# Kernel optimization log

Measured on AMD Instinct MI355X. Metric: run time of the kernel, lower is better.

The kernel has to match this reference:

```python
import jax, jax.numpy as jnp
import numpy as np

CUTOFF = 5.0

def ssp(x):
    # shifted softplus: ln(0.5*e^x + 0.5)
    return jax.nn.softplus(x) - jnp.log(2.0).astype(x.dtype)

def cosine_cutoff(r):
    return 0.5 * (jnp.cos(jnp.pi * r / CUTOFF) + 1.0) * (r < CUTOFF).astype(r.dtype)

def setup_inputs() -> dict:
    key = jax.random.key(0)
    ks = jax.random.split(key, 16)
    B, A, N, Nd, F, Din, Dout, Th = 2, 512, 1024, 64, 64, 128, 128, 25
    inp = {}
    inp['x'] = jax.random.normal(ks[0], (B, A, Din), dtype=jnp.float32)
    inp['r_double'] = jax.random.uniform(ks[1], (B, A, Nd), dtype=jnp.float32)
    inp['r_ij'] = jax.random.uniform(ks[2], (B, A, N), dtype=jnp.float32)
    inp['r_ik'] = jax.random.uniform(ks[3], (B, A, N), dtype=jnp.float32)
    inp['r_jk'] = jax.random.uniform(ks[4], (B, A, N), dtype=jnp.float32)
    inp['neighbors'] = jax.random.randint(ks[5], (B, A, Nd), 0, A, dtype=jnp.int32)
    inp['neighbor_mask'] = jnp.ones((B, A, Nd), dtype=jnp.float32)
    inp['neighbors_j'] = jax.random.randint(ks[6], (B, A, N), 0, A, dtype=jnp.int32)
    inp['neighbors_k'] = jax.random.randint(ks[7], (B, A, N), 0, A, dtype=jnp.int32)
    inp['triple_masks'] = jnp.ones((B, A, N), dtype=jnp.float32)
    inp['d_ijk'] = jax.random.uniform(ks[8], (B, A, N, Th), dtype=jnp.float32)
    s = 0.1
    inp['W_in2f'] = s * jax.random.normal(ks[9], (Din, F), dtype=jnp.float32)
    inp['W_t1'] = s * jax.random.normal(ks[10], (Th, F), dtype=jnp.float32)
    inp['b_t1'] = jnp.zeros((F,), dtype=jnp.float32)
    inp['W_t2'] = s * jax.random.normal(ks[11], (F, F), dtype=jnp.float32)
    inp['b_t2'] = jnp.zeros((F,), dtype=jnp.float32)
    inp['W_f2out'] = s * jax.random.normal(ks[12], (F, Dout), dtype=jnp.float32)
    inp['b_f2out'] = jnp.zeros((Dout,), dtype=jnp.float32)
    return inp

def reference(x, r_double, r_ij, r_ik, r_jk, neighbors, neighbor_mask,
              neighbors_j, neighbors_k, triple_masks, d_ijk,
              W_in2f, W_t1, b_t1, W_t2, b_t2, W_f2out, b_f2out):
    # Triple filter: 2-layer MLP on angular basis, modulated by cutoffs
    h = ssp(jnp.einsum('bant,tf->banf', d_ijk, W_t1) + b_t1)
    W_triple = jnp.einsum('banf,fg->bang', h, W_t2) + b_t2
    W_triple = W_triple * cosine_cutoff(r_ij)[..., None] * cosine_cutoff(r_ik)[..., None]

    # in2f: (B, A, F)
    y = jnp.einsum('bad,df->baf', x, W_in2f)
    B, A, N = neighbors_j.shape
    F = y.shape[-1]
    # gather neighbor features along atom axis
    yj = jnp.take_along_axis(y, neighbors_j.reshape(B, A * N, 1), axis=1).reshape(B, A, N, F)
    yk = jnp.take_along_axis(y, neighbors_k.reshape(B, A * N, 1), axis=1).reshape(B, A, N, F)
    w_ij = r_ij[..., None]
    w_ik = r_ik[..., None]
    y = (w_ij * yj + w_ik * yk) / (w_ij + w_ik)
    # filter multiply + masked sum aggregation over triples axis
    y = y * W_triple
    y = jnp.sum(y * triple_masks[..., None], axis=2)
    # f2out with shifted-softplus activation
    out = ssp(jnp.einsum('baf,fo->bao', y, W_f2out) + b_f2out)
    return out
```

## Files before the change

### kernel.cpp

```cpp
#include <hip/hip_runtime.h>
#include <hip/hip_fp16.h>

#define BB 2
#define AA 512
#define NN 1024
#define FF 64
#define DIN 128
#define DOUT 128
#define TH 25
#define ASTRIDE 40
#define HSTRIDE 72
#define NSPLIT 4

typedef _Float16 half8 __attribute__((ext_vector_type(8)));
typedef _Float16 half4v __attribute__((ext_vector_type(4)));
typedef float floatx4 __attribute__((ext_vector_type(4)));

__device__ __forceinline__ float ssp_f(float x) {
    return __logf(0.5f * __expf(x) + 0.5f);
}

__device__ __forceinline__ float cutcos(float r) {
    float c = 0.5f * (__cosf(r * (3.14159265358979323846f / 5.0f)) + 1.0f);
    return (r < 5.0f) ? c : 0.0f;
}

__device__ __forceinline__ __half2 ssp2(__half2 x) {
    const __half2 hlf = __float2half2_rn(0.5f);
    return h2log(__hfma2(h2exp(x), hlf, hlf));
}

__device__ __forceinline__ __half2 pk2(float a, float b) {
    auto v = __builtin_amdgcn_cvt_pkrtz(a, b);
    __half2 r;
    __builtin_memcpy(&r, &v, sizeof(r));
    return r;
}

__device__ __forceinline__ half4v pack4(__half2 lo, __half2 hi) {
    half4v r;
    __builtin_memcpy(&r, &lo, 4);
    __builtin_memcpy(reinterpret_cast<char*>(&r) + 4, &hi, 4);
    return r;
}

#define OFF_Y       0
#define OFF_PARTIAL (OFF_Y + (size_t)BB * AA * FF * 2)
#define OFF_B1      (OFF_PARTIAL + (size_t)NSPLIT * BB * AA * FF * 4)
#define OFF_B2      (OFF_B1 + 4 * 64 * 8 * 2)
#define OFF_BP      (OFF_B2 + 8 * 64 * 8 * 2)

__global__ void in2f_prep_kernel(const float* __restrict__ x,
                                 const float* __restrict__ Wi,
                                 _Float16* __restrict__ y,
                                 const float* __restrict__ W_t1, const float* __restrict__ b_t1,
                                 const float* __restrict__ W_t2, const float* __restrict__ b_t2,
                                 _Float16* __restrict__ B1tab, _Float16* __restrict__ B2tab,
                                 _Float16* __restrict__ BPtab) {
    __shared__ float xs[DIN];
    const int ba = blockIdx.x;
    const int t = threadIdx.x;
    xs[t] = x[ba * DIN + t];
    xs[t + 64] = x[ba * DIN + 64 + t];
    __syncthreads();
    float acc = 0.f;
#pragma unroll 8
    for (int d = 0; d < DIN; ++d) acc += xs[d] * Wi[d * FF + t];
    y[ba * FF + t] = (_Float16)acc;

    if (ba == 0) {
        const int lane = t, quad = t >> 4, l16 = t & 15;
#pragma unroll
        for (int g = 0; g < 4; ++g) {
#pragma unroll
            for (int j = 0; j < 8; ++j) {
                int k = quad * 8 + j;
                B1tab[(g * 64 + lane) * 8 + j] =
                    (k < TH) ? (_Float16)W_t1[k * FF + g * 16 + l16] : (_Float16)0.f;
            }
#pragma unroll
            for (int e = 0; e < 2; ++e) {
                BPtab[((g * 2 + e) * 64 + lane) * 2 + 0] =
                    (_Float16)b_t1[g * 16 + quad * 4 + 2 * e];
                BPtab[((g * 2 + e) * 64 + lane) * 2 + 1] =
                    (_Float16)b_t1[g * 16 + quad * 4 + 2 * e + 1];
                BPtab[1024 + ((g * 2 + e) * 64 + lane) * 2 + 0] =
                    (_Float16)b_t2[g * 16 + quad * 4 + 2 * e];
                BPtab[1024 + ((g * 2 + e) * 64 + lane) * 2 + 1] =
                    (_Float16)b_t2[g * 16 + quad * 4 + 2 * e + 1];
            }
#pragma unroll
            for (int q = 0; q < 2; ++q)
#pragma unroll
                for (int j = 0; j < 8; ++j)
                    B2tab[((g * 2 + q) * 64 + lane) * 8 + j] =
                        (_Float16)W_t2[(q * 32 + quad * 8 + j) * FF + g * 16 + l16];
        }
    }
}

__global__ __launch_bounds__(256) void triple_kernel(
    const int* __restrict__ nbrj, const int* __restrict__ nbrk,
    const float* __restrict__ r_ij, const float* __restrict__ r_ik,
    const float* __restrict__ tmask, const float* __restrict__ d_ijk,
    const _Float16* __restrict__ B1tab, const _Float16* __restrict__ B2tab,
    const _Float16* __restrict__ BPtab,
    const _Float16* __restrict__ y_tab, float* __restrict__ partial) {

    __shared__ __align__(16) _Float16 a_tile[4][16 * ASTRIDE];
    __shared__ __align__(16) _Float16 h_tile[4][16 * HSTRIDE];
    __shared__ float red[4][FF];

    const int blk = blockIdx.x;
    const int ba = blk >> 2;
    const int split = blk & 3;
    const int b = ba >> 9;
    const int tid = threadIdx.x;
    const int w = tid >> 6;
    const int lane = tid & 63;
    const int quad = lane >> 4;
    const int l16 = lane & 15;
    const int rA = lane >> 3;
    const int fc = (lane & 7) * 8;

    const long ban = (long)ba * NN;
    const float* dbase = d_ijk + (long)ba * NN * TH;
    const _Float16* yb = y_tab + (long)b * (AA * FF);

    half8 B1[4];
    half8 B2[4][2];
    __half2 b1p[4][2], b2p[4][2];
#pragma unroll
    for (int g = 0; g < 4; ++g) {
        B1[g] = *(const half8*)(B1tab + (g * 64 + lane) * 8);
        B2[g][0] = *(const half8*)(B2tab + ((g * 2 + 0) * 64 + lane) * 8);
        B2[g][1] = *(const half8*)(B2tab + ((g * 2 + 1) * 64 + lane) * 8);
#pragma unroll
        for (int e = 0; e < 2; ++e) {
            b1p[g][e] = *(const __half2*)(BPtab + ((g * 2 + e) * 64 + lane) * 2);
            b2p[g][e] = *(const __half2*)(BPtab + 1024 + ((g * 2 + e) * 64 + lane) * 2);
        }
    }

    const int myn = (split * 16 + quad * 4 + w) * 16 + l16;
    const long myna = ban + myn;
    const float rijL = r_ij[myna], rikL = r_ik[myna];
    const float ivL = cutcos(rijL) * cutcos(rikL) * tmask[myna] / (rijL + rikL);
    const float wjf = rijL * ivL, wkf = rikL * ivL;
    const int pjL = nbrj[myna], pkL = nbrk[myna];

    for (int idx = lane; idx < 16 * 7; idx += 64) {
        int r = idx / 7, c = 25 + idx % 7;
        a_tile[w][r * ASTRIDE + c] = (_Float16)0.f;
    }

    int lofs2[3][2];
#pragma unroll
    for (int m = 0; m < 3; ++m)
#pragma unroll
        for (int e = 0; e < 2; ++e) {
            int s = m * 128 + lane * 2 + e;
            int r = s / TH, c = s - r * TH;
            lofs2[m][e] = r * ASTRIDE + c;
        }
    const int tofs = 15 * ASTRIDE + 9 + lane;

    float acc[8];
#pragma unroll
    for (int i = 0; i < 8; ++i) acc[i] = 0.f;
    const floatx4 zero4 = {0.f, 0.f, 0.f, 0.f};

    float2 pA[3];
    float pT = 0.f;
    {
        const int n0 = (split * 16 + w) * 16;
        const float* dsrc = dbase + n0 * TH;
#pragma unroll
        for (int m = 0; m < 3; ++m) pA[m] = *(const float2*)(dsrc + m * 128 + lane * 2);
        if (lane < 16) pT = dsrc[384 + lane];
    }

#pragma unroll 1
    for (int it = 0; it < NN / (16 * 4 * NSPLIT); ++it) {
        const int sl0 = it * 16 + rA;
        const int sl1 = sl0 + 8;
        const int pj0 = __shfl(pjL, sl0), pk0 = __shfl(pkL, sl0);
        const int pj1 = __shfl(pjL, sl1), pk1 = __shfl(pkL, sl1);
        half8 gj0 = *(const half8*)(yb + pj0 * FF + fc);
        half8 gk0 = *(const half8*)(yb + pk0 * FF + fc);
        half8 gj1 = *(const half8*)(yb + pj1 * FF + fc);
        half8 gk1 = *(const half8*)(yb + pk1 * FF + fc);

#pragma unroll
        for (int m = 0; m < 3; ++m) {
            a_tile[w][lofs2[m][0]] = (_Float16)pA[m].x;
            a_tile[w][lofs2[m][1]] = (_Float16)pA[m].y;
        }
        if (lane < 16) a_tile[w][tofs] = (_Float16)pT;

        if (it + 1 < NN / (16 * 4 * NSPLIT)) {
            const int n0 = (split * 16 + (it + 1) * 4 + w) * 16;
            const float* dn = dbase + n0 * TH;
#pragma unroll
            for (int m = 0; m < 3; ++m) pA[m] = *(const float2*)(dn + m * 128 + lane * 2);
            if (lane < 16) pT = dn[384 + lane];
        }

        const __half2 wj0 = __float2half2_rn(__shfl(wjf, sl0));
        const __half2 wk0 = __float2half2_rn(__shfl(wkf, sl0));
        const __half2 wj1 = __float2half2_rn(__shfl(wjf, sl1));
        const __half2 wk1 = __float2half2_rn(__shfl(wkf, sl1));

        half8 afrag = *(const half8*)&a_tile[w][l16 * ASTRIDE + quad * 8];
#pragma unroll
        for (int g = 0; g < 4; ++g) {
            floatx4 hv = __builtin_amdgcn_mfma_f32_16x16x32_f16(B1[g], afrag, zero4, 0, 0, 0);
            __half2 h01 = ssp2(__hadd2(pk2(hv[0], hv[1]), b1p[g][0]));
            __half2 h23 = ssp2(__hadd2(pk2(hv[2], hv[3]), b1p[g][1]));
            *(half4v*)&h_tile[w][l16 * HSTRIDE + g * 16 + quad * 4] = pack4(h01, h23);
        }

        half8 a2q0 = *(const half8*)&h_tile[w][l16 * HSTRIDE + quad * 8];
        half8 a2q1 = *(const half8*)&h_tile[w][l16 * HSTRIDE + 32 + quad * 8];
#pragma unroll
        for (int g = 0; g < 4; ++g) {
            floatx4 w2 = __builtin_amdgcn_mfma_f32_16x16x32_f16(B2[g][0], a2q0, zero4, 0, 0, 0);
            w2 = __builtin_amdgcn_mfma_f32_16x16x32_f16(B2[g][1], a2q1, w2, 0, 0, 0);
            __half2 f01 = __hadd2(pk2(w2[0], w2[1]), b2p[g][0]);
            __half2 f23 = __hadd2(pk2(w2[2], w2[3]), b2p[g][1]);
            *(half4v*)&h_tile[w][l16 * HSTRIDE + g * 16 + quad * 4] = pack4(f01, f23);
        }
        half8 f0 = *(const half8*)&h_tile[w][rA * HSTRIDE + fc];
        half8 f1 = *(const half8*)&h_tile[w][(8 + rA) * HSTRIDE + fc];

        const __half2* gj0p = (const __half2*)&gj0;
        const __half2* gk0p = (const __half2*)&gk0;
        const __half2* gj1p = (const __half2*)&gj1;
        const __half2* gk1p = (const __half2*)&gk1;
        const __half2* f0p = (const __half2*)&f0;
        const __half2* f1p = (const __half2*)&f1;
#pragma unroll
        for (int p = 0; p < 4; ++p) {
            __half2 fv0 = __hfma2(wj0, gj0p[p], __hmul2(wk0, gk0p[p]));
            __half2 fv1 = __hfma2(wj1, gj1p[p], __hmul2(wk1, gk1p[p]));
            __half2 tot = __hfma2(f1p[p], fv1, __hmul2(f0p[p], fv0));
            acc[2 * p]     += __low2float(tot);
            acc[2 * p + 1] += __high2float(tot);
        }
    }

#pragma unroll
    for (int i = 0; i < 8; ++i) {
        acc[i] += __shfl_xor(acc[i], 8, 64);
        acc[i] += __shfl_xor(acc[i], 16, 64);
        acc[i] += __shfl_xor(acc[i], 32, 64);
    }
    if (lane < 8)
#pragma unroll
        for (int i = 0; i < 8; ++i) red[w][lane * 8 + i] = acc[i];
    __syncthreads();

    if (tid < FF)
        partial[(split * (BB * AA) + ba) * FF + tid] =
            red[0][tid] + red[1][tid] + red[2][tid] + red[3][tid];
}

__global__ void out_kernel(const float* __restrict__ partial,
                           const float* __restrict__ Wf,
                           const float* __restrict__ bf,
                           float* __restrict__ out) {
    __shared__ float yag[FF];
    const int ba = blockIdx.x;
    const int t = threadIdx.x;
    if (t < FF) {
        float s = 0.f;
#pragma unroll
        for (int sp = 0; sp < NSPLIT; ++sp)
            s += partial[(sp * (BB * AA) + ba) * FF + t];
        yag[t] = s;
    }
    __syncthreads();
    float a = bf[t];
#pragma unroll 8
    for (int f = 0; f < FF; ++f) a += yag[f] * Wf[f * DOUT + t];
    out[(long)ba * DOUT + t] = ssp_f(a);
}

extern "C" void kernel_launch(void* const* d_in, const int* in_sizes, int n_in,
                              void* d_out, int out_size, void* d_ws, size_t ws_size,
                              hipStream_t stream) {
    const float* x       = (const float*)d_in[0];
    const float* r_ij    = (const float*)d_in[2];
    const float* r_ik    = (const float*)d_in[3];
    const int*   nbrj    = (const int*)d_in[7];
    const int*   nbrk    = (const int*)d_in[8];
    const float* tmask   = (const float*)d_in[9];
    const float* d_ijk   = (const float*)d_in[10];
    const float* W_in2f  = (const float*)d_in[11];
    const float* W_t1    = (const float*)d_in[12];
    const float* b_t1    = (const float*)d_in[13];
    const float* W_t2    = (const float*)d_in[14];
    const float* b_t2    = (const float*)d_in[15];
    const float* W_f2out = (const float*)d_in[16];
    const float* b_f2out = (const float*)d_in[17];
    float* out = (float*)d_out;

    char* ws = (char*)d_ws;
    _Float16* y      = (_Float16*)(ws + OFF_Y);
    float* partial   = (float*)(ws + OFF_PARTIAL);
    _Float16* B1tab  = (_Float16*)(ws + OFF_B1);
    _Float16* B2tab  = (_Float16*)(ws + OFF_B2);
    _Float16* BPtab  = (_Float16*)(ws + OFF_BP);

    in2f_prep_kernel<<<BB * AA, 64, 0, stream>>>(x, W_in2f, y, W_t1, b_t1,
                                                 W_t2, b_t2, B1tab, B2tab, BPtab);
    triple_kernel<<<BB * AA * NSPLIT, 256, 0, stream>>>(nbrj, nbrk, r_ij, r_ik,
                                                        tmask, d_ijk, B1tab, B2tab,
                                                        BPtab, y, partial);
    out_kernel<<<BB * AA, 128, 0, stream>>>(partial, W_f2out, b_f2out, out);
}
```

Measured before the change: 239.1 us.

## Keep MFMA fragments in registers, removing LDS staging of MLP tiles

The first-layer weight columns are permuted so that the MFMA output fragment of layer one directly forms the B-operand fragment of layer two. This lets the hidden activations stay in registers instead of round-tripping through LDS tiles. The d_ijk input is loaded straight from global memory into the A fragment, and neighbor gathers use the MFMA output layout so the filter multiply happens in fp32 per lane. The loop is fully unrolled with double-buffered prefetch, at the cost of more registers and a longer shuffle reduction.

```diff
diff --git a/kernel.cpp b/kernel.cpp
--- a/kernel.cpp
+++ b/kernel.cpp
@@ -8,9 +8,8 @@
 #define DIN 128
 #define DOUT 128
 #define TH 25
-#define ASTRIDE 40
-#define HSTRIDE 72
 #define NSPLIT 4
+#define NIT 4
 
 typedef _Float16 half8 __attribute__((ext_vector_type(8)));
 typedef _Float16 half4v __attribute__((ext_vector_type(4)));
@@ -37,10 +36,12 @@
     return r;
 }
 
-__device__ __forceinline__ half4v pack4(__half2 lo, __half2 hi) {
-    half4v r;
-    __builtin_memcpy(&r, &lo, 4);
-    __builtin_memcpy(reinterpret_cast<char*>(&r) + 4, &hi, 4);
+__device__ __forceinline__ half8 pack8(__half2 a, __half2 b, __half2 c, __half2 d) {
+    half8 r;
+    __builtin_memcpy(reinterpret_cast<char*>(&r) + 0,  &a, 4);
+    __builtin_memcpy(reinterpret_cast<char*>(&r) + 4,  &b, 4);
+    __builtin_memcpy(reinterpret_cast<char*>(&r) + 8,  &c, 4);
+    __builtin_memcpy(reinterpret_cast<char*>(&r) + 12, &d, 4);
     return r;
 }
 
@@ -48,7 +49,8 @@
 #define OFF_PARTIAL (OFF_Y + (size_t)BB * AA * FF * 2)
 #define OFF_B1      (OFF_PARTIAL + (size_t)NSPLIT * BB * AA * FF * 4)
 #define OFF_B2      (OFF_B1 + 4 * 64 * 8 * 2)
-#define OFF_BP      (OFF_B2 + 8 * 64 * 8 * 2)
+#define OFF_B1P     (OFF_B2 + 8 * 64 * 8 * 2)
+#define OFF_B2F     (OFF_B1P + 4 * 2 * 64 * 2 * 2)
 
 __global__ void in2f_prep_kernel(const float* __restrict__ x,
                                  const float* __restrict__ Wi,
@@ -56,7 +58,7 @@
                                  const float* __restrict__ W_t1, const float* __restrict__ b_t1,
                                  const float* __restrict__ W_t2, const float* __restrict__ b_t2,
                                  _Float16* __restrict__ B1tab, _Float16* __restrict__ B2tab,
-                                 _Float16* __restrict__ BPtab) {
+                                 _Float16* __restrict__ B1Ptab, float* __restrict__ B2Ftab) {
     __shared__ float xs[DIN];
     const int ba = blockIdx.x;
     const int t = threadIdx.x;
@@ -70,24 +72,22 @@
 
     if (ba == 0) {
         const int lane = t, quad = t >> 4, l16 = t & 15;
-#pragma unroll
-        for (int g = 0; g < 4; ++g) {
+        const int baseg[4] = {0, 4, 32, 36};
+#pragma unroll
+        for (int g = 0; g < 4; ++g) {
+            const int feat_m = baseg[g] + 8 * (l16 >> 2) + (l16 & 3);
 #pragma unroll
             for (int j = 0; j < 8; ++j) {
                 int k = quad * 8 + j;
                 B1tab[(g * 64 + lane) * 8 + j] =
-                    (k < TH) ? (_Float16)W_t1[k * FF + g * 16 + l16] : (_Float16)0.f;
+                    (k < TH) ? (_Float16)W_t1[k * FF + feat_m] : (_Float16)0.f;
             }
 #pragma unroll
             for (int e = 0; e < 2; ++e) {
-                BPtab[((g * 2 + e) * 64 + lane) * 2 + 0] =
-                    (_Float16)b_t1[g * 16 + quad * 4 + 2 * e];
-                BPtab[((g * 2 + e) * 64 + lane) * 2 + 1] =
-                    (_Float16)b_t1[g * 16 + quad * 4 + 2 * e + 1];
-                BPtab[1024 + ((g * 2 + e) * 64 + lane) * 2 + 0] =
-                    (_Float16)b_t2[g * 16 + quad * 4 + 2 * e];
-                BPtab[1024 + ((g * 2 + e) * 64 + lane) * 2 + 1] =
-                    (_Float16)b_t2[g * 16 + quad * 4 + 2 * e + 1];
+                B1Ptab[((g * 2 + e) * 64 + lane) * 2 + 0] =
+                    (_Float16)b_t1[baseg[g] + 8 * quad + 2 * e];
+                B1Ptab[((g * 2 + e) * 64 + lane) * 2 + 1] =
+                    (_Float16)b_t1[baseg[g] + 8 * quad + 2 * e + 1];
             }
 #pragma unroll
             for (int q = 0; q < 2; ++q)
@@ -95,6 +95,9 @@
                 for (int j = 0; j < 8; ++j)
                     B2tab[((g * 2 + q) * 64 + lane) * 8 + j] =
                         (_Float16)W_t2[(q * 32 + quad * 8 + j) * FF + g * 16 + l16];
+#pragma unroll
+            for (int r = 0; r < 4; ++r)
+                B2Ftab[lane * 16 + g * 4 + r] = b_t2[g * 16 + 4 * quad + r];
         }
     }
 }
@@ -104,12 +107,10 @@
     const float* __restrict__ r_ij, const float* __restrict__ r_ik,
     const float* __restrict__ tmask, const float* __restrict__ d_ijk,
     const _Float16* __restrict__ B1tab, const _Float16* __restrict__ B2tab,
-    const _Float16* __restrict__ BPtab,
+    const _Float16* __restrict__ B1Ptab, const float* __restrict__ B2Ftab,
     const _Float16* __restrict__ y_tab, float* __restrict__ partial) {
 
-    __shared__ __align__(16) _Float16 a_tile[4][16 * ASTRIDE];
-    __shared__ __align__(16) _Float16 h_tile[4][16 * HSTRIDE];
-    __shared__ float red[4][FF];
+    __shared__ __align__(16) float red[4][FF];
 
     const int blk = blockIdx.x;
     const int ba = blk >> 2;
@@ -120,8 +121,6 @@
     const int lane = tid & 63;
     const int quad = lane >> 4;
     const int l16 = lane & 15;
-    const int rA = lane >> 3;
-    const int fc = (lane & 7) * 8;
 
     const long ban = (long)ba * NN;
     const float* dbase = d_ijk + (long)ba * NN * TH;
@@ -129,135 +128,118 @@
 
     half8 B1[4];
     half8 B2[4][2];
-    __half2 b1p[4][2], b2p[4][2];
+    __half2 b1p[4][2];
+    floatx4 b2f[4];
 #pragma unroll
     for (int g = 0; g < 4; ++g) {
         B1[g] = *(const half8*)(B1tab + (g * 64 + lane) * 8);
         B2[g][0] = *(const half8*)(B2tab + ((g * 2 + 0) * 64 + lane) * 8);
         B2[g][1] = *(const half8*)(B2tab + ((g * 2 + 1) * 64 + lane) * 8);
-#pragma unroll
-        for (int e = 0; e < 2; ++e) {
-            b1p[g][e] = *(const __half2*)(BPtab + ((g * 2 + e) * 64 + lane) * 2);
-            b2p[g][e] = *(const __half2*)(BPtab + 1024 + ((g * 2 + e) * 64 + lane) * 2);
-        }
+        b1p[g][0] = *(const __half2*)(B1Ptab + ((g * 2 + 0) * 64 + lane) * 2);
+        b1p[g][1] = *(const __half2*)(B1Ptab + ((g * 2 + 1) * 64 + lane) * 2);
+        b2f[g] = *(const floatx4*)(B2Ftab + lane * 16 + g * 4);
     }
 
     const int myn = (split * 16 + quad * 4 + w) * 16 + l16;
     const long myna = ban + myn;
     const float rijL = r_ij[myna], rikL = r_ik[myna];
     const float ivL = cutcos(rijL) * cutcos(rikL) * tmask[myna] / (rijL + rikL);
-    const float wjf = rijL * ivL, wkf = rikL * ivL;
+    const float wjL = rijL * ivL, wkL = rikL * ivL;
     const int pjL = nbrj[myna], pkL = nbrk[myna];
 
-    for (int idx = lane; idx < 16 * 7; idx += 64) {
-        int r = idx / 7, c = 25 + idx % 7;
-        a_tile[w][r * ASTRIDE + c] = (_Float16)0.f;
-    }
-
-    int lofs2[3][2];
-#pragma unroll
-    for (int m = 0; m < 3; ++m)
-#pragma unroll
-        for (int e = 0; e < 2; ++e) {
-            int s = m * 128 + lane * 2 + e;
-            int r = s / TH, c = s - r * TH;
-            lofs2[m][e] = r * ASTRIDE + c;
-        }
-    const int tofs = 15 * ASTRIDE + 9 + lane;
-
-    float acc[8];
-#pragma unroll
-    for (int i = 0; i < 8; ++i) acc[i] = 0.f;
+    const float* dp0 = dbase + (long)((split * 16 + w) * 16 + l16) * TH + quad * 8;
+    const bool qok = (quad < 3);
+
+    float acc[16];
+#pragma unroll
+    for (int i = 0; i < 16; ++i) acc[i] = 0.f;
     const floatx4 zero4 = {0.f, 0.f, 0.f, 0.f};
 
-    float2 pA[3];
-    float pT = 0.f;
+    float dv[2][8];
+    half4v gj[2][4], gk[2][4];
+    float wjc[2], wkc[2];
+
     {
-        const int n0 = (split * 16 + w) * 16;
-        const float* dsrc = dbase + n0 * TH;
-#pragma unroll
-        for (int m = 0; m < 3; ++m) pA[m] = *(const float2*)(dsrc + m * 128 + lane * 2);
-        if (lane < 16) pT = dsrc[384 + lane];
-    }
-
-#pragma unroll 1
-    for (int it = 0; it < NN / (16 * 4 * NSPLIT); ++it) {
-        const int sl0 = it * 16 + rA;
-        const int sl1 = sl0 + 8;
-        const int pj0 = __shfl(pjL, sl0), pk0 = __shfl(pkL, sl0);
-        const int pj1 = __shfl(pjL, sl1), pk1 = __shfl(pkL, sl1);
-        half8 gj0 = *(const half8*)(yb + pj0 * FF + fc);
-        half8 gk0 = *(const half8*)(yb + pk0 * FF + fc);
-        half8 gj1 = *(const half8*)(yb + pj1 * FF + fc);
-        half8 gk1 = *(const half8*)(yb + pk1 * FF + fc);
-
-#pragma unroll
-        for (int m = 0; m < 3; ++m) {
-            a_tile[w][lofs2[m][0]] = (_Float16)pA[m].x;
-            a_tile[w][lofs2[m][1]] = (_Float16)pA[m].y;
-        }
-        if (lane < 16) a_tile[w][tofs] = (_Float16)pT;
-
-        if (it + 1 < NN / (16 * 4 * NSPLIT)) {
-            const int n0 = (split * 16 + (it + 1) * 4 + w) * 16;
-            const float* dn = dbase + n0 * TH;
-#pragma unroll
-            for (int m = 0; m < 3; ++m) pA[m] = *(const float2*)(dn + m * 128 + lane * 2);
-            if (lane < 16) pT = dn[384 + lane];
-        }
-
-        const __half2 wj0 = __float2half2_rn(__shfl(wjf, sl0));
-        const __half2 wk0 = __float2half2_rn(__shfl(wkf, sl0));
-        const __half2 wj1 = __float2half2_rn(__shfl(wjf, sl1));
-        const __half2 wk1 = __float2half2_rn(__shfl(wkf, sl1));
-
-        half8 afrag = *(const half8*)&a_tile[w][l16 * ASTRIDE + quad * 8];
-#pragma unroll
-        for (int g = 0; g < 4; ++g) {
-            floatx4 hv = __builtin_amdgcn_mfma_f32_16x16x32_f16(B1[g], afrag, zero4, 0, 0, 0);
-            __half2 h01 = ssp2(__hadd2(pk2(hv[0], hv[1]), b1p[g][0]));
-            __half2 h23 = ssp2(__hadd2(pk2(hv[2], hv[3]), b1p[g][1]));
-            *(half4v*)&h_tile[w][l16 * HSTRIDE + g * 16 + quad * 4] = pack4(h01, h23);
-        }
-
-        half8 a2q0 = *(const half8*)&h_tile[w][l16 * HSTRIDE + quad * 8];
-        half8 a2q1 = *(const half8*)&h_tile[w][l16 * HSTRIDE + 32 + quad * 8];
+        const int sl = l16;
+        const int pj = __shfl(pjL, sl), pk = __shfl(pkL, sl);
+        wjc[0] = __shfl(wjL, sl);
+        wkc[0] = __shfl(wkL, sl);
+        const _Float16* pjb = yb + pj * FF + quad * 4;
+        const _Float16* pkb = yb + pk * FF + quad * 4;
+#pragma unroll
+        for (int g = 0; g < 4; ++g) {
+            gj[0][g] = *(const half4v*)(pjb + g * 16);
+            gk[0][g] = *(const half4v*)(pkb + g * 16);
+        }
+        dv[0][0] = dp0[0];
+#pragma unroll
+        for (int j = 1; j < 8; ++j) dv[0][j] = qok ? dp0[j] : 0.f;
+    }
+
+#pragma unroll
+    for (int it = 0; it < NIT; ++it) {
+        const int cur = it & 1, nxt = cur ^ 1;
+
+        if (it + 1 < NIT) {
+            const int sl = (it + 1) * 16 + l16;
+            const int pj = __shfl(pjL, sl), pk = __shfl(pkL, sl);
+            wjc[nxt] = __shfl(wjL, sl);
+            wkc[nxt] = __shfl(wkL, sl);
+            const _Float16* pjb = yb + pj * FF + quad * 4;
+            const _Float16* pkb = yb + pk * FF + quad * 4;
+#pragma unroll
+            for (int g = 0; g < 4; ++g) {
+                gj[nxt][g] = *(const half4v*)(pjb + g * 16);
+                gk[nxt][g] = *(const half4v*)(pkb + g * 16);
+            }
+            const float* dp = dp0 + (it + 1) * 1600;
+            dv[nxt][0] = dp[0];
+#pragma unroll
+            for (int j = 1; j < 8; ++j) dv[nxt][j] = qok ? dp[j] : 0.f;
+        }
+
+        const half8 af = pack8(pk2(dv[cur][0], dv[cur][1]), pk2(dv[cur][2], dv[cur][3]),
+                               pk2(dv[cur][4], dv[cur][5]), pk2(dv[cur][6], dv[cur][7]));
+
+        __half2 hh[8];
+#pragma unroll
+        for (int g = 0; g < 4; ++g) {
+            floatx4 hv = __builtin_amdgcn_mfma_f32_16x16x32_f16(B1[g], af, zero4, 0, 0, 0);
+            hh[2 * g]     = ssp2(__hadd2(pk2(hv[0], hv[1]), b1p[g][0]));
+            hh[2 * g + 1] = ssp2(__hadd2(pk2(hv[2], hv[3]), b1p[g][1]));
+        }
+        const half8 a2q0 = pack8(hh[0], hh[1], hh[2], hh[3]);
+        const half8 a2q1 = pack8(hh[4], hh[5], hh[6], hh[7]);
+
+        const __half2 wjh = __float2half2_rn(wjc[cur]);
+        const __half2 wkh = __float2half2_rn(wkc[cur]);
 #pragma unroll
         for (int g = 0; g < 4; ++g) {
             floatx4 w2 = __builtin_amdgcn_mfma_f32_16x16x32_f16(B2[g][0], a2q0, zero4, 0, 0, 0);
             w2 = __builtin_amdgcn_mfma_f32_16x16x32_f16(B2[g][1], a2q1, w2, 0, 0, 0);
-            __half2 f01 = __hadd2(pk2(w2[0], w2[1]), b2p[g][0]);
-            __half2 f23 = __hadd2(pk2(w2[2], w2[3]), b2p[g][1]);
-            *(half4v*)&h_tile[w][l16 * HSTRIDE + g * 16 + quad * 4] = pack4(f01, f23);
-        }
-        half8 f0 = *(const half8*)&h_tile[w][rA * HSTRIDE + fc];
-        half8 f1 = *(const half8*)&h_tile[w][(8 + rA) * HSTRIDE + fc];
-
-        const __half2* gj0p = (const __half2*)&gj0;
-        const __half2* gk0p = (const __half2*)&gk0;
-        const __half2* gj1p = (const __half2*)&gj1;
-        const __half2* gk1p = (const __half2*)&gk1;
-        const __half2* f0p = (const __half2*)&f0;
-        const __half2* f1p = (const __half2*)&f1;
-#pragma unroll
-        for (int p = 0; p < 4; ++p) {
-            __half2 fv0 = __hfma2(wj0, gj0p[p], __hmul2(wk0, gk0p[p]));
-            __half2 fv1 = __hfma2(wj1, gj1p[p], __hmul2(wk1, gk1p[p]));
-            __half2 tot = __hfma2(f1p[p], fv1, __hmul2(f0p[p], fv0));
-            acc[2 * p]     += __low2float(tot);
-            acc[2 * p + 1] += __high2float(tot);
-        }
-    }
-
-#pragma unroll
-    for (int i = 0; i < 8; ++i) {
-        acc[i] += __shfl_xor(acc[i], 8, 64);
-        acc[i] += __shfl_xor(acc[i], 16, 64);
-        acc[i] += __shfl_xor(acc[i], 32, 64);
-    }
-    if (lane < 8)
-#pragma unroll
-        for (int i = 0; i < 8; ++i) red[w][lane * 8 + i] = acc[i];
+            const __half2* yjp = (const __half2*)&gj[cur][g];
+            const __half2* ykp = (const __half2*)&gk[cur][g];
+            const __half2 fv0 = __hfma2(wjh, yjp[0], __hmul2(wkh, ykp[0]));
+            const __half2 fv1 = __hfma2(wjh, yjp[1], __hmul2(wkh, ykp[1]));
+            acc[g * 4 + 0] += (w2[0] + b2f[g][0]) * __low2float(fv0);
+            acc[g * 4 + 1] += (w2[1] + b2f[g][1]) * __high2float(fv0);
+            acc[g * 4 + 2] += (w2[2] + b2f[g][2]) * __low2float(fv1);
+            acc[g * 4 + 3] += (w2[3] + b2f[g][3]) * __high2float(fv1);
+        }
+    }
+
+#pragma unroll
+    for (int m = 1; m < 16; m <<= 1)
+#pragma unroll
+        for (int i = 0; i < 16; ++i) acc[i] += __shfl_xor(acc[i], m, 64);
+
+    if (l16 == 0) {
+#pragma unroll
+        for (int g = 0; g < 4; ++g) {
+            floatx4 v = {acc[g * 4 + 0], acc[g * 4 + 1], acc[g * 4 + 2], acc[g * 4 + 3]};
+            *(floatx4*)&red[w][g * 16 + quad * 4] = v;
+        }
+    }
     __syncthreads();
 
     if (tid < FF)
@@ -310,12 +292,14 @@
     float* partial   = (float*)(ws + OFF_PARTIAL);
     _Float16* B1tab  = (_Float16*)(ws + OFF_B1);
     _Float16* B2tab  = (_Float16*)(ws + OFF_B2);
-    _Float16* BPtab  = (_Float16*)(ws + OFF_BP);
+    _Float16* B1Ptab = (_Float16*)(ws + OFF_B1P);
+    float* B2Ftab    = (float*)(ws + OFF_B2F);
 
     in2f_prep_kernel<<<BB * AA, 64, 0, stream>>>(x, W_in2f, y, W_t1, b_t1,
-                                                 W_t2, b_t2, B1tab, B2tab, BPtab);
+                                                 W_t2, b_t2, B1tab, B2tab,
+                                                 B1Ptab, B2Ftab);
     triple_kernel<<<BB * AA * NSPLIT, 256, 0, stream>>>(nbrj, nbrk, r_ij, r_ik,
                                                         tmask, d_ijk, B1tab, B2tab,
-                                                        BPtab, y, partial);
+                                                        B1Ptab, B2Ftab, y, partial);
     out_kernel<<<BB * AA, 128, 0, stream>>>(partial, W_f2out, b_f2out, out);
 }
```

Result: slower. 277.6 us (+16.1%).

## Process two triple tiles per iteration and keep hidden layer in registers

Applied to the files above, without the earlier changes.

The main loop is unrolled by two: each iteration handles two 16-triple tiles with double-buffered LDS tiles and separate accumulators, so twice as many gathers and MFMAs are in flight. The first-layer weight columns are permuted so the MFMA output layout matches the A-operand layout of the second MFMA. This lets the ssp hidden activations be packed straight into registers instead of going through an LDS round trip. The cost is higher register and LDS pressure, which may lower occupancy.

```diff
diff --git a/kernel.cpp b/kernel.cpp
--- a/kernel.cpp
+++ b/kernel.cpp
@@ -11,6 +11,7 @@
 #define ASTRIDE 40
 #define HSTRIDE 72
 #define NSPLIT 4
+#define NIT 4
 
 typedef _Float16 half8 __attribute__((ext_vector_type(8)));
 typedef _Float16 half4v __attribute__((ext_vector_type(4)));
@@ -41,6 +42,15 @@
     half4v r;
     __builtin_memcpy(&r, &lo, 4);
     __builtin_memcpy(reinterpret_cast<char*>(&r) + 4, &hi, 4);
+    return r;
+}
+
+__device__ __forceinline__ half8 pack8(__half2 a, __half2 b, __half2 c, __half2 d) {
+    half8 r;
+    __builtin_memcpy(reinterpret_cast<char*>(&r) + 0,  &a, 4);
+    __builtin_memcpy(reinterpret_cast<char*>(&r) + 4,  &b, 4);
+    __builtin_memcpy(reinterpret_cast<char*>(&r) + 8,  &c, 4);
+    __builtin_memcpy(reinterpret_cast<char*>(&r) + 12, &d, 4);
     return r;
 }
 
@@ -70,20 +80,22 @@
 
     if (ba == 0) {
         const int lane = t, quad = t >> 4, l16 = t & 15;
+        const int baseg[4] = {0, 4, 32, 36};
 #pragma unroll
         for (int g = 0; g < 4; ++g) {
+            const int feat_m = baseg[g] + 8 * (l16 >> 2) + (l16 & 3);
 #pragma unroll
             for (int j = 0; j < 8; ++j) {
                 int k = quad * 8 + j;
                 B1tab[(g * 64 + lane) * 8 + j] =
-                    (k < TH) ? (_Float16)W_t1[k * FF + g * 16 + l16] : (_Float16)0.f;
+                    (k < TH) ? (_Float16)W_t1[k * FF + feat_m] : (_Float16)0.f;
             }
 #pragma unroll
             for (int e = 0; e < 2; ++e) {
                 BPtab[((g * 2 + e) * 64 + lane) * 2 + 0] =
-                    (_Float16)b_t1[g * 16 + quad * 4 + 2 * e];
+                    (_Float16)b_t1[baseg[g] + 8 * quad + 2 * e];
                 BPtab[((g * 2 + e) * 64 + lane) * 2 + 1] =
-                    (_Float16)b_t1[g * 16 + quad * 4 + 2 * e + 1];
+                    (_Float16)b_t1[baseg[g] + 8 * quad + 2 * e + 1];
                 BPtab[1024 + ((g * 2 + e) * 64 + lane) * 2 + 0] =
                     (_Float16)b_t2[g * 16 + quad * 4 + 2 * e];
                 BPtab[1024 + ((g * 2 + e) * 64 + lane) * 2 + 1] =
@@ -107,8 +119,8 @@
     const _Float16* __restrict__ BPtab,
     const _Float16* __restrict__ y_tab, float* __restrict__ partial) {
 
-    __shared__ __align__(16) _Float16 a_tile[4][16 * ASTRIDE];
-    __shared__ __align__(16) _Float16 h_tile[4][16 * HSTRIDE];
+    __shared__ __align__(16) _Float16 a_tile[4][2][16 * ASTRIDE];
+    __shared__ __align__(16) _Float16 f_tile[4][2][16 * HSTRIDE];
     __shared__ float red[4][FF];
 
     const int blk = blockIdx.x;
@@ -146,12 +158,13 @@
     const long myna = ban + myn;
     const float rijL = r_ij[myna], rikL = r_ik[myna];
     const float ivL = cutcos(rijL) * cutcos(rikL) * tmask[myna] / (rijL + rikL);
-    const float wjf = rijL * ivL, wkf = rikL * ivL;
+    const float wjL = rijL * ivL, wkL = rikL * ivL;
     const int pjL = nbrj[myna], pkL = nbrk[myna];
 
     for (int idx = lane; idx < 16 * 7; idx += 64) {
         int r = idx / 7, c = 25 + idx % 7;
-        a_tile[w][r * ASTRIDE + c] = (_Float16)0.f;
+        a_tile[w][0][r * ASTRIDE + c] = (_Float16)0.f;
+        a_tile[w][1][r * ASTRIDE + c] = (_Float16)0.f;
     }
 
     int lofs2[3][2];
@@ -165,99 +178,158 @@
         }
     const int tofs = 15 * ASTRIDE + 9 + lane;
 
-    float acc[8];
-#pragma unroll
-    for (int i = 0; i < 8; ++i) acc[i] = 0.f;
+    float acc0[8], acc1[8];
+#pragma unroll
+    for (int i = 0; i < 8; ++i) { acc0[i] = 0.f; acc1[i] = 0.f; }
     const floatx4 zero4 = {0.f, 0.f, 0.f, 0.f};
 
-    float2 pA[3];
-    float pT = 0.f;
+    float2 pA0[3], pA1[3];
+    float pT0 = 0.f, pT1 = 0.f;
     {
         const int n0 = (split * 16 + w) * 16;
-        const float* dsrc = dbase + n0 * TH;
-#pragma unroll
-        for (int m = 0; m < 3; ++m) pA[m] = *(const float2*)(dsrc + m * 128 + lane * 2);
-        if (lane < 16) pT = dsrc[384 + lane];
+        const float* d0 = dbase + (long)n0 * TH;
+        const float* d1 = d0 + 4 * 16 * TH;
+#pragma unroll
+        for (int m = 0; m < 3; ++m) {
+            pA0[m] = *(const float2*)(d0 + m * 128 + lane * 2);
+            pA1[m] = *(const float2*)(d1 + m * 128 + lane * 2);
+        }
+        if (lane < 16) { pT0 = d0[384 + lane]; pT1 = d1[384 + lane]; }
     }
 
 #pragma unroll 1
-    for (int it = 0; it < NN / (16 * 4 * NSPLIT); ++it) {
-        const int sl0 = it * 16 + rA;
-        const int sl1 = sl0 + 8;
-        const int pj0 = __shfl(pjL, sl0), pk0 = __shfl(pkL, sl0);
-        const int pj1 = __shfl(pjL, sl1), pk1 = __shfl(pkL, sl1);
-        half8 gj0 = *(const half8*)(yb + pj0 * FF + fc);
-        half8 gk0 = *(const half8*)(yb + pk0 * FF + fc);
-        half8 gj1 = *(const half8*)(yb + pj1 * FF + fc);
-        half8 gk1 = *(const half8*)(yb + pk1 * FF + fc);
+    for (int pit = 0; pit < NIT / 2; ++pit) {
+        const int t0 = pit * 2, t1 = t0 + 1;
+
+        const int sa0 = t0 * 16 + rA, sa1 = sa0 + 8;
+        const int sb0 = t1 * 16 + rA, sb1 = sb0 + 8;
+        const int pja0 = __shfl(pjL, sa0), pka0 = __shfl(pkL, sa0);
+        const int pja1 = __shfl(pjL, sa1), pka1 = __shfl(pkL, sa1);
+        const int pjb0 = __shfl(pjL, sb0), pkb0 = __shfl(pkL, sb0);
+        const int pjb1 = __shfl(pjL, sb1), pkb1 = __shfl(pkL, sb1);
+        half8 gja0 = *(const half8*)(yb + pja0 * FF + fc);
+        half8 gka0 = *(const half8*)(yb + pka0 * FF + fc);
+        half8 gja1 = *(const half8*)(yb + pja1 * FF + fc);
+        half8 gka1 = *(const half8*)(yb + pka1 * FF + fc);
+        half8 gjb0 = *(const half8*)(yb + pjb0 * FF + fc);
+        half8 gkb0 = *(const half8*)(yb + pkb0 * FF + fc);
+        half8 gjb1 = *(const half8*)(yb + pjb1 * FF + fc);
+        half8 gkb1 = *(const half8*)(yb + pkb1 * FF + fc);
 
 #pragma unroll
         for (int m = 0; m < 3; ++m) {
-            a_tile[w][lofs2[m][0]] = (_Float16)pA[m].x;
-            a_tile[w][lofs2[m][1]] = (_Float16)pA[m].y;
-        }
-        if (lane < 16) a_tile[w][tofs] = (_Float16)pT;
-
-        if (it + 1 < NN / (16 * 4 * NSPLIT)) {
-            const int n0 = (split * 16 + (it + 1) * 4 + w) * 16;
-            const float* dn = dbase + n0 * TH;
-#pragma unroll
-            for (int m = 0; m < 3; ++m) pA[m] = *(const float2*)(dn + m * 128 + lane * 2);
-            if (lane < 16) pT = dn[384 + lane];
-        }
-
-        const __half2 wj0 = __float2half2_rn(__shfl(wjf, sl0));
-        const __half2 wk0 = __float2half2_rn(__shfl(wkf, sl0));
-        const __half2 wj1 = __float2half2_rn(__shfl(wjf, sl1));
-        const __half2 wk1 = __float2half2_rn(__shfl(wkf, sl1));
-
-        half8 afrag = *(const half8*)&a_tile[w][l16 * ASTRIDE + quad * 8];
+            a_tile[w][0][lofs2[m][0]] = (_Float16)pA0[m].x;
+            a_tile[w][0][lofs2[m][1]] = (_Float16)pA0[m].y;
+            a_tile[w][1][lofs2[m][0]] = (_Float16)pA1[m].x;
+            a_tile[w][1][lofs2[m][1]] = (_Float16)pA1[m].y;
+        }
+        if (lane < 16) {
+            a_tile[w][0][tofs] = (_Float16)pT0;
+            a_tile[w][1][tofs] = (_Float16)pT1;
+        }
+
+        if (pit + 1 < NIT / 2) {
+            const int n0 = (split * 16 + (t0 + 2) * 4 + w) * 16;
+            const float* d0 = dbase + (long)n0 * TH;
+            const float* d1 = d0 + 4 * 16 * TH;
+#pragma unroll
+            for (int m = 0; m < 3; ++m) {
+                pA0[m] = *(const float2*)(d0 + m * 128 + lane * 2);
+                pA1[m] = *(const float2*)(d1 + m * 128 + lane * 2);
+            }
+            if (lane < 16) { pT0 = d0[384 + lane]; pT1 = d1[384 + lane]; }
+        }
+
+        const __half2 wja0 = __float2half2_rn(__shfl(wjL, sa0));
+        const __half2 wka0 = __float2half2_rn(__shfl(wkL, sa0));
+        const __half2 wja1 = __float2half2_rn(__shfl(wjL, sa1));
+        const __half2 wka1 = __float2half2_rn(__shfl(wkL, sa1));
+        const __half2 wjb0 = __float2half2_rn(__shfl(wjL, sb0));
+        const __half2 wkb0 = __float2half2_rn(__shfl(wkL, sb0));
+        const __half2 wjb1 = __float2half2_rn(__shfl(wjL, sb1));
+        const __half2 wkb1 = __float2half2_rn(__shfl(wkL, sb1));
+
+        half8 afA = *(const half8*)&a_tile[w][0][l16 * ASTRIDE + quad * 8];
+        half8 afB = *(const half8*)&a_tile[w][1][l16 * ASTRIDE + quad * 8];
+        __half2 hhA[8], hhB[8];
 #pragma unroll
         for (int g = 0; g < 4; ++g) {
-            floatx4 hv = __builtin_amdgcn_mfma_f32_16x16x32_f16(B1[g], afrag, zero4, 0, 0, 0);
-            __half2 h01 = ssp2(__hadd2(pk2(hv[0], hv[1]), b1p[g][0]));
-            __half2 h23 = ssp2(__hadd2(pk2(hv[2], hv[3]), b1p[g][1]));
-            *(half4v*)&h_tile[w][l16 * HSTRIDE + g * 16 + quad * 4] = pack4(h01, h23);
-        }
-
-        half8 a2q0 = *(const half8*)&h_tile[w][l16 * HSTRIDE + quad * 8];
-        half8 a2q1 = *(const half8*)&h_tile[w][l16 * HSTRIDE + 32 + quad * 8];
+            floatx4 hvA = __builtin_amdgcn_mfma_f32_16x16x32_f16(B1[g], afA, zero4, 0, 0, 0);
+            floatx4 hvB = __builtin_amdgcn_mfma_f32_16x16x32_f16(B1[g], afB, zero4, 0, 0, 0);
+            hhA[2 * g]     = ssp2(__hadd2(pk2(hvA[0], hvA[1]), b1p[g][0]));
+            hhB[2 * g]     = ssp2(__hadd2(pk2(hvB[0], hvB[1]), b1p[g][0]));
+            hhA[2 * g + 1] = ssp2(__hadd2(pk2(hvA[2], hvA[3]), b1p[g][1]));
+            hhB[2 * g + 1] = ssp2(__hadd2(pk2(hvB[2], hvB[3]), b1p[g][1]));
+        }
+        const half8 a2A0 = pack8(hhA[0], hhA[1], hhA[2], hhA[3]);
+        const half8 a2A1 = pack8(hhA[4], hhA[5], hhA[6], hhA[7]);
+        const half8 a2B0 = pack8(hhB[0], hhB[1], hhB[2], hhB[3]);
+        const half8 a2B1 = pack8(hhB[4], hhB[5], hhB[6], hhB[7]);
+
 #pragma unroll
         for (int g = 0; g < 4; ++g) {
-            floatx4 w2 = __builtin_amdgcn_mfma_f32_16x16x32_f16(B2[g][0], a2q0, zero4, 0, 0, 0);
-            w2 = __builtin_amdgcn_mfma_f32_16x16x32_f16(B2[g][1], a2q1, w2, 0, 0, 0);
-            __half2 f01 = __hadd2(pk2(w2[0], w2[1]), b2p[g][0]);
-            __half2 f23 = __hadd2(pk2(w2[2], w2[3]), b2p[g][1]);
-            *(half4v*)&h_tile[w][l16 * HSTRIDE + g * 16 + quad * 4] = pack4(f01, f23);
-        }
-        half8 f0 = *(const half8*)&h_tile[w][rA * HSTRIDE + fc];
-        half8 f1 = *(const half8*)&h_tile[w][(8 + rA) * HSTRIDE + fc];
-
-        const __half2* gj0p = (const __half2*)&gj0;
-        const __half2* gk0p = (const __half2*)&gk0;
-        const __half2* gj1p = (const __half2*)&gj1;
-        const __half2* gk1p = (const __half2*)&gk1;
-        const __half2* f0p = (const __half2*)&f0;
-        const __half2* f1p = (const __half2*)&f1;
-#pragma unroll
-        for (int p = 0; p < 4; ++p) {
-            __half2 fv0 = __hfma2(wj0, gj0p[p], __hmul2(wk0, gk0p[p]));
-            __half2 fv1 = __hfma2(wj1, gj1p[p], __hmul2(wk1, gk1p[p]));
-            __half2 tot = __hfma2(f1p[p], fv1, __hmul2(f0p[p], fv0));
-            acc[2 * p]     += __low2float(tot);
-            acc[2 * p + 1] += __high2float(tot);
-        }
-    }
-
+            floatx4 w2A = __builtin_amdgcn_mfma_f32_16x16x32_f16(B2[g][0], a2A0, zero4, 0, 0, 0);
+            floatx4 w2B = __builtin_amdgcn_mfma_f32_16x16x32_f16(B2[g][0], a2B0, zero4, 0, 0, 0);
+            w2A = __builtin_amdgcn_mfma_f32_16x16x32_f16(B2[g][1], a2A1, w2A, 0, 0, 0);
+            w2B = __builtin_amdgcn_mfma_f32_16x16x32_f16(B2[g][1], a2B1, w2B, 0, 0, 0);
+            __half2 fA01 = __hadd2(pk2(w2A[0], w2A[1]), b2p[g][0]);
+            __half2 fA23 = __hadd2(pk2(w2A[2], w2A[3]), b2p[g][1]);
+            __half2 fB01 = __hadd2(pk2(w2B[0], w2B[1]), b2p[g][0]);
+            __half2 fB23 = __hadd2(pk2(w2B[2], w2B[3]), b2p[g][1]);
+            *(half4v*)&f_tile[w][0][l16 * HSTRIDE + g * 16 + quad * 4] = pack4(fA01, fA23);
+            *(half4v*)&f_tile[w][1][l16 * HSTRIDE + g * 16 + quad * 4] = pack4(fB01, fB23);
+        }
+        half8 f0A = *(const half8*)&f_tile[w][0][rA * HSTRIDE + fc];
+        half8 f1A = *(const half8*)&f_tile[w][0][(8 + rA) * HSTRIDE + fc];
+        half8 f0B = *(const half8*)&f_tile[w][1][rA * HSTRIDE + fc];
+        half8 f1B = *(const half8*)&f_tile[w][1][(8 + rA) * HSTRIDE + fc];
+
+        {
+            const __half2* gj0p = (const __half2*)&gja0;
+            const __half2* gk0p = (const __half2*)&gka0;
+            const __half2* gj1p = (const __half2*)&gja1;
+            const __half2* gk1p = (const __half2*)&gka1;
+            const __half2* f0p = (const __half2*)&f0A;
+            const __half2* f1p = (const __half2*)&f1A;
+#pragma unroll
+            for (int p = 0; p < 4; ++p) {
+                __half2 fv0 = __hfma2(wja0, gj0p[p], __hmul2(wka0, gk0p[p]));
+                __half2 fv1 = __hfma2(wja1, gj1p[p], __hmul2(wka1, gk1p[p]));
+                __half2 tot = __hfma2(f1p[p], fv1, __hmul2(f0p[p], fv0));
+                acc0[2 * p]     += __low2float(tot);
+                acc0[2 * p + 1] += __high2float(tot);
+            }
+        }
+        {
+            const __half2* gj0p = (const __half2*)&gjb0;
+            const __half2* gk0p = (const __half2*)&gkb0;
+            const __half2* gj1p = (const __half2*)&gjb1;
+            const __half2* gk1p = (const __half2*)&gkb1;
+            const __half2* f0p = (const __half2*)&f0B;
+            const __half2* f1p = (const __half2*)&f1B;
+#pragma unroll
+            for (int p = 0; p < 4; ++p) {
+                __half2 fv0 = __hfma2(wjb0, gj0p[p], __hmul2(wkb0, gk0p[p]));
+                __half2 fv1 = __hfma2(wjb1, gj1p[p], __hmul2(wkb1, gk1p[p]));
+                __half2 tot = __hfma2(f1p[p], fv1, __hmul2(f0p[p], fv0));
+                acc1[2 * p]     += __low2float(tot);
+                acc1[2 * p + 1] += __high2float(tot);
+            }
+        }
+    }
+
+    float accr[8];
 #pragma unroll
     for (int i = 0; i < 8; ++i) {
-        acc[i] += __shfl_xor(acc[i], 8, 64);
-        acc[i] += __shfl_xor(acc[i], 16, 64);
-        acc[i] += __shfl_xor(acc[i], 32, 64);
+        float a = acc0[i] + acc1[i];
+        a += __shfl_xor(a, 8, 64);
+        a += __shfl_xor(a, 16, 64);
+        a += __shfl_xor(a, 32, 64);
+        accr[i] = a;
     }
     if (lane < 8)
 #pragma unroll
-        for (int i = 0; i < 8; ++i) red[w][lane * 8 + i] = acc[i];
+        for (int i = 0; i < 8; ++i) red[w][lane * 8 + i] = accr[i];
     __syncthreads();
 
     if (tid < FF)
```

After: 248.2 us. 1.04x slower.

## Fold bias and exp/log base change into MFMA weights, double split count

Applied to the files above, without the earlier changes.

Folds b_t1 into the first MFMA through a constant-one column in the A tile, pre-scaled by log2(e) with the 0.5 factor absorbed as -1. Softplus then runs on exp2/log2, and ln2 is folded into W_t2. This removes the per-element bias add and the fma in the activation. The triples axis is split 8 ways instead of 4, giving twice as many blocks with half the iterations each, which raises parallelism but adds partial-sum reduction work.

```diff
diff --git a/kernel.cpp b/kernel.cpp
--- a/kernel.cpp
+++ b/kernel.cpp
@@ -10,12 +10,16 @@
 #define TH 25
 #define ASTRIDE 40
 #define HSTRIDE 72
-#define NSPLIT 4
+#define NSPLIT 8
+#define NIT 2
 
 typedef _Float16 half8 __attribute__((ext_vector_type(8)));
 typedef _Float16 half4v __attribute__((ext_vector_type(4)));
 typedef float floatx4 __attribute__((ext_vector_type(4)));
 
+#define LOG2E 1.44269504088896f
+#define LN2F  0.693147180559945f
+
 __device__ __forceinline__ float ssp_f(float x) {
     return __logf(0.5f * __expf(x) + 0.5f);
 }
@@ -25,9 +29,9 @@
     return (r < 5.0f) ? c : 0.0f;
 }
 
-__device__ __forceinline__ __half2 ssp2(__half2 x) {
+__device__ __forceinline__ __half2 ssp2f(__half2 z) {
     const __half2 hlf = __float2half2_rn(0.5f);
-    return h2log(__hfma2(h2exp(x), hlf, hlf));
+    return h2log2(__hadd2(h2exp2(z), hlf));
 }
 
 __device__ __forceinline__ __half2 pk2(float a, float b) {
@@ -72,21 +76,21 @@
         const int lane = t, quad = t >> 4, l16 = t & 15;
 #pragma unroll
         for (int g = 0; g < 4; ++g) {
+            const int featA = g * 16 + l16;
 #pragma unroll
             for (int j = 0; j < 8; ++j) {
                 int k = quad * 8 + j;
-                B1tab[(g * 64 + lane) * 8 + j] =
-                    (k < TH) ? (_Float16)W_t1[k * FF + g * 16 + l16] : (_Float16)0.f;
+                _Float16 v;
+                if (k < TH)       v = (_Float16)(W_t1[k * FF + featA] * LOG2E);
+                else if (k == TH) v = (_Float16)(b_t1[featA] * LOG2E - 1.0f);
+                else              v = (_Float16)0.f;
+                B1tab[(g * 64 + lane) * 8 + j] = v;
             }
 #pragma unroll
             for (int e = 0; e < 2; ++e) {
                 BPtab[((g * 2 + e) * 64 + lane) * 2 + 0] =
-                    (_Float16)b_t1[g * 16 + quad * 4 + 2 * e];
+                    (_Float16)b_t2[g * 16 + quad * 4 + 2 * e];
                 BPtab[((g * 2 + e) * 64 + lane) * 2 + 1] =
-                    (_Float16)b_t1[g * 16 + quad * 4 + 2 * e + 1];
-                BPtab[1024 + ((g * 2 + e) * 64 + lane) * 2 + 0] =
-                    (_Float16)b_t2[g * 16 + quad * 4 + 2 * e];
-                BPtab[1024 + ((g * 2 + e) * 64 + lane) * 2 + 1] =
                     (_Float16)b_t2[g * 16 + quad * 4 + 2 * e + 1];
             }
 #pragma unroll
@@ -94,7 +98,7 @@
 #pragma unroll
                 for (int j = 0; j < 8; ++j)
                     B2tab[((g * 2 + q) * 64 + lane) * 8 + j] =
-                        (_Float16)W_t2[(q * 32 + quad * 8 + j) * FF + g * 16 + l16];
+                        (_Float16)(W_t2[(q * 32 + quad * 8 + j) * FF + g * 16 + l16] * LN2F);
         }
     }
 }
@@ -112,8 +116,8 @@
     __shared__ float red[4][FF];
 
     const int blk = blockIdx.x;
-    const int ba = blk >> 2;
-    const int split = blk & 3;
+    const int ba = blk >> 3;
+    const int split = blk & 7;
     const int b = ba >> 9;
     const int tid = threadIdx.x;
     const int w = tid >> 6;
@@ -129,29 +133,27 @@
 
     half8 B1[4];
     half8 B2[4][2];
-    __half2 b1p[4][2], b2p[4][2];
+    __half2 b2p[4][2];
 #pragma unroll
     for (int g = 0; g < 4; ++g) {
         B1[g] = *(const half8*)(B1tab + (g * 64 + lane) * 8);
         B2[g][0] = *(const half8*)(B2tab + ((g * 2 + 0) * 64 + lane) * 8);
         B2[g][1] = *(const half8*)(B2tab + ((g * 2 + 1) * 64 + lane) * 8);
 #pragma unroll
-        for (int e = 0; e < 2; ++e) {
-            b1p[g][e] = *(const __half2*)(BPtab + ((g * 2 + e) * 64 + lane) * 2);
-            b2p[g][e] = *(const __half2*)(BPtab + 1024 + ((g * 2 + e) * 64 + lane) * 2);
-        }
-    }
-
-    const int myn = (split * 16 + quad * 4 + w) * 16 + l16;
+        for (int e = 0; e < 2; ++e)
+            b2p[g][e] = *(const __half2*)(BPtab + ((g * 2 + e) * 64 + lane) * 2);
+    }
+
+    const int myn = (split * 8 + (quad & 1) * 4 + w) * 16 + l16;
     const long myna = ban + myn;
     const float rijL = r_ij[myna], rikL = r_ik[myna];
     const float ivL = cutcos(rijL) * cutcos(rikL) * tmask[myna] / (rijL + rikL);
-    const float wjf = rijL * ivL, wkf = rikL * ivL;
+    const float wjL = rijL * ivL, wkL = rikL * ivL;
     const int pjL = nbrj[myna], pkL = nbrk[myna];
 
     for (int idx = lane; idx < 16 * 7; idx += 64) {
         int r = idx / 7, c = 25 + idx % 7;
-        a_tile[w][r * ASTRIDE + c] = (_Float16)0.f;
+        a_tile[w][r * ASTRIDE + c] = (c == 25) ? (_Float16)1.f : (_Float16)0.f;
     }
 
     int lofs2[3][2];
@@ -173,15 +175,15 @@
     float2 pA[3];
     float pT = 0.f;
     {
-        const int n0 = (split * 16 + w) * 16;
-        const float* dsrc = dbase + n0 * TH;
+        const int n0 = (split * 8 + w) * 16;
+        const float* dsrc = dbase + (long)n0 * TH;
 #pragma unroll
         for (int m = 0; m < 3; ++m) pA[m] = *(const float2*)(dsrc + m * 128 + lane * 2);
         if (lane < 16) pT = dsrc[384 + lane];
     }
 
 #pragma unroll 1
-    for (int it = 0; it < NN / (16 * 4 * NSPLIT); ++it) {
+    for (int it = 0; it < NIT; ++it) {
         const int sl0 = it * 16 + rA;
         const int sl1 = sl0 + 8;
         const int pj0 = __shfl(pjL, sl0), pk0 = __shfl(pkL, sl0);
@@ -198,25 +200,25 @@
         }
         if (lane < 16) a_tile[w][tofs] = (_Float16)pT;
 
-        if (it + 1 < NN / (16 * 4 * NSPLIT)) {
-            const int n0 = (split * 16 + (it + 1) * 4 + w) * 16;
-            const float* dn = dbase + n0 * TH;
+        if (it + 1 < NIT) {
+            const int n0 = (split * 8 + (it + 1) * 4 + w) * 16;
+            const float* dn = dbase + (long)n0 * TH;
 #pragma unroll
             for (int m = 0; m < 3; ++m) pA[m] = *(const float2*)(dn + m * 128 + lane * 2);
             if (lane < 16) pT = dn[384 + lane];
         }
 
-        const __half2 wj0 = __float2half2_rn(__shfl(wjf, sl0));
-        const __half2 wk0 = __float2half2_rn(__shfl(wkf, sl0));
-        const __half2 wj1 = __float2half2_rn(__shfl(wjf, sl1));
-        const __half2 wk1 = __float2half2_rn(__shfl(wkf, sl1));
+        const __half2 wj0 = __float2half2_rn(__shfl(wjL, sl0));
+        const __half2 wk0 = __float2half2_rn(__shfl(wkL, sl0));
+        const __half2 wj1 = __float2half2_rn(__shfl(wjL, sl1));
+        const __half2 wk1 = __float2half2_rn(__shfl(wkL, sl1));
 
         half8 afrag = *(const half8*)&a_tile[w][l16 * ASTRIDE + quad * 8];
 #pragma unroll
         for (int g = 0; g < 4; ++g) {
             floatx4 hv = __builtin_amdgcn_mfma_f32_16x16x32_f16(B1[g], afrag, zero4, 0, 0, 0);
-            __half2 h01 = ssp2(__hadd2(pk2(hv[0], hv[1]), b1p[g][0]));
-            __half2 h23 = ssp2(__hadd2(pk2(hv[2], hv[3]), b1p[g][1]));
+            __half2 h01 = ssp2f(pk2(hv[0], hv[1]));
+            __half2 h23 = ssp2f(pk2(hv[2], hv[3]));
             *(half4v*)&h_tile[w][l16 * HSTRIDE + g * 16 + quad * 4] = pack4(h01, h23);
         }
 
```

Result: slower. 246.1 us (+2.9%).
